# Kernel tuning notes

Hardware: AMD Instinct MI355X
Metric: run time of the kernel (lower is better)

The kernel has to match this reference:

```python
import jax, jax.numpy as jnp
import numpy as np

TROPICAL_ZERO = jnp.float32(-1e38)  # tropical additive identity (acts as -inf)


def setup_inputs() -> dict:
    key = jax.random.key(0)
    k_x, k_w = jax.random.split(key)
    B, IN, OUT = 4096, 256, 256
    x = jax.random.normal(k_x, (B, IN), dtype=jnp.float32)
    # weight = log(rand + 1e-6), matching nn.Parameter init in the torch module
    weight = jnp.log(jax.random.uniform(k_w, (OUT, IN), dtype=jnp.float32) + 1e-6)
    bias = jnp.zeros((OUT,), dtype=jnp.float32)
    return {"x": x, "weight": weight, "bias": bias}


def reference(x, weight, bias):
    # Tropical (max-plus) matmul: out[b, j] = max_k (x[b, k] + w[j, k]) + bias[j]
    # restricted to 'non-tropical-zero' products; if all products are tropical
    # zero, the output stays TROPICAL_ZERO (no bias added), as in the torch loop.
    products = x[:, None, :] + weight[None, :, :]          # [B, out, in]
    mask = products > TROPICAL_ZERO                        # [B, out, in]
    masked = jnp.where(mask, products, -jnp.inf)
    max_val = jnp.max(masked, axis=-1)                     # [B, out]
    any_valid = jnp.any(mask, axis=-1)                     # [B, out]
    out = jnp.where(any_valid, max_val + bias[None, :], TROPICAL_ZERO)
    return out
```

## Files before the change

kernel.cpp:

```cpp
#include <hip/hip_runtime.h>


#define TZERO -1e38f

constexpr int K     = 256;
constexpr int N     = 256;
constexpr int RPW   = 4;
constexpr int WAVES = 4;
constexpr int BM    = RPW * WAVES;
constexpr int BN    = 64;
constexpr int NT    = 64 * WAVES;
constexpr int BK    = 64;
constexpr int NC    = K / BK;
constexpr int K4C   = BK / 4;

__global__ __launch_bounds__(NT, 4)
void tropical_kernel(const float* __restrict__ x, const float* __restrict__ w,
                     const float* __restrict__ bias, float* __restrict__ out)
{
    __shared__ float4 wQ[2][K4C][BN];

    const int t    = threadIdx.x;
    const int lane = t & 63;
    const int wave = __builtin_amdgcn_readfirstlane(t >> 6);
    const int row0 = blockIdx.x * BM + wave * RPW;
    const int col0 = blockIdx.y * BN;

    const int scol = t & 63;
    const int sq   = t >> 6;
    const float* wsrc = w + (size_t)(col0 + scol) * K + sq * 16;

#pragma unroll
    for (int i = 0; i < 4; ++i)
        wQ[0][sq * 4 + i][scol] =
            *reinterpret_cast<const float4*>(wsrc + i * 4);
    __syncthreads();

    const float* xw = x + (size_t)row0 * K;

    float acc[RPW];
#pragma unroll
    for (int r = 0; r < RPW; ++r) acc[r] = -__builtin_inff();

    for (int c = 0; c < NC; ++c) {
        if (c + 1 < NC) {
            const float* ws = wsrc + (c + 1) * BK;
#pragma unroll
            for (int i = 0; i < 4; ++i)
                wQ[(c + 1) & 1][sq * 4 + i][scol] =
                    *reinterpret_cast<const float4*>(ws + i * 4);
        }

        const float* xc = xw + c * BK;
#pragma unroll 8
        for (int k4 = 0; k4 < K4C; ++k4) {
            const float4 wv = wQ[c & 1][k4][lane];
#pragma unroll
            for (int r = 0; r < RPW; ++r) {
                const float4 xv =
                    *reinterpret_cast<const float4*>(xc + r * K + k4 * 4);
                const float t0 = xv.x + wv.x;
                const float t1 = xv.y + wv.y;
                const float t2 = xv.z + wv.z;
                const float t3 = xv.w + wv.w;
                float m = fmaxf(fmaxf(acc[r], t0), t1);
                m       = fmaxf(fmaxf(m, t2), t3);
                acc[r] = m;
            }
        }
        __syncthreads();
    }

    const float bj = bias[col0 + lane];
    float* orow = out + (size_t)row0 * N + col0 + lane;
#pragma unroll
    for (int r = 0; r < RPW; ++r) {
        const float v = acc[r];
        orow[(size_t)r * N] = (v > TZERO) ? v + bj : TZERO;
    }
}

extern "C" void kernel_launch(void* const* d_in, const int* in_sizes, int n_in,
                              void* d_out, int out_size, void* d_ws, size_t ws_size,
                              hipStream_t stream) {
    const float* x  = (const float*)d_in[0];
    const float* w  = (const float*)d_in[1];
    const float* b  = (const float*)d_in[2];
    float* out      = (float*)d_out;

    dim3 grid(4096 / BM, N / BN);
    tropical_kernel<<<grid, NT, 0, stream>>>(x, w, b, out);
}
```

Before: 71.80 us.

## Split K across waves with register-resident weights and LDS max reduction

Each of the four waves now owns a quarter of the K dimension and keeps its 64-wide weight slice in registers (16 float4), instead of streaming weight chunks through double-buffered LDS. Each wave processes all 16 rows of the block, and the partial maxima are combined through a small shared array after one barrier. Two independent max chains per row add instruction-level parallelism. This removes the per-chunk LDS weight traffic and barriers, but costs higher register pressure (64 VGPRs for weights) and extra LDS work for the cross-wave reduction.

```diff
diff --git a/kernel.cpp b/kernel.cpp
--- a/kernel.cpp
+++ b/kernel.cpp
@@ -3,80 +3,65 @@
 
 #define TZERO -1e38f
 
-constexpr int K     = 256;
-constexpr int N     = 256;
-constexpr int RPW   = 4;
-constexpr int WAVES = 4;
-constexpr int BM    = RPW * WAVES;
-constexpr int BN    = 64;
-constexpr int NT    = 64 * WAVES;
-constexpr int BK    = 64;
-constexpr int NC    = K / BK;
-constexpr int K4C   = BK / 4;
+constexpr int K    = 256;
+constexpr int N    = 256;
+constexpr int ROWS = 16;
+constexpr int NT   = 256;
 
 __global__ __launch_bounds__(NT, 4)
 void tropical_kernel(const float* __restrict__ x, const float* __restrict__ w,
                      const float* __restrict__ bias, float* __restrict__ out)
 {
-    __shared__ float4 wQ[2][K4C][BN];
+    __shared__ float part[4][ROWS][64];
 
     const int t    = threadIdx.x;
     const int lane = t & 63;
-    const int wave = __builtin_amdgcn_readfirstlane(t >> 6);
-    const int row0 = blockIdx.x * BM + wave * RPW;
-    const int col0 = blockIdx.y * BN;
+    const int kq   = __builtin_amdgcn_readfirstlane(t >> 6);
+    const int row0 = blockIdx.x * ROWS;
+    const int col0 = blockIdx.y * 64;
 
-    const int scol = t & 63;
-    const int sq   = t >> 6;
-    const float* wsrc = w + (size_t)(col0 + scol) * K + sq * 16;
+    const float* wsrc = w + (size_t)(col0 + lane) * K + kq * 64;
+    float4 wq[16];
+#pragma unroll
+    for (int i = 0; i < 16; ++i)
+        wq[i] = *reinterpret_cast<const float4*>(wsrc + 4 * i);
 
+    const float bj = bias[col0 + lane];
+
+    const float* xbase = x + (size_t)row0 * K + kq * 64;
+
+#pragma unroll 2
+    for (int r = 0; r < ROWS; ++r) {
+        const float* xr = xbase + (size_t)r * K;
+        float m0 = -__builtin_inff();
+        float m1 = -__builtin_inff();
 #pragma unroll
-    for (int i = 0; i < 4; ++i)
-        wQ[0][sq * 4 + i][scol] =
-            *reinterpret_cast<const float4*>(wsrc + i * 4);
+        for (int i = 0; i < 16; ++i) {
+            const float4 xv = *reinterpret_cast<const float4*>(xr + 4 * i);
+            const float t0 = xv.x + wq[i].x;
+            const float t1 = xv.y + wq[i].y;
+            const float t2 = xv.z + wq[i].z;
+            const float t3 = xv.w + wq[i].w;
+            if (i & 1) {
+                m1 = fmaxf(fmaxf(m1, t0), t1);
+                m1 = fmaxf(fmaxf(m1, t2), t3);
+            } else {
+                m0 = fmaxf(fmaxf(m0, t0), t1);
+                m0 = fmaxf(fmaxf(m0, t2), t3);
+            }
+        }
+        part[kq][r][lane] = fmaxf(m0, m1);
+    }
+
     __syncthreads();
 
-    const float* xw = x + (size_t)row0 * K;
-
-    float acc[RPW];
+    const int er0 = (t >> 6) * 4;
 #pragma unroll
-    for (int r = 0; r < RPW; ++r) acc[r] = -__builtin_inff();
-
-    for (int c = 0; c < NC; ++c) {
-        if (c + 1 < NC) {
-            const float* ws = wsrc + (c + 1) * BK;
-#pragma unroll
-            for (int i = 0; i < 4; ++i)
-                wQ[(c + 1) & 1][sq * 4 + i][scol] =
-                    *reinterpret_cast<const float4*>(ws + i * 4);
-        }
-
-        const float* xc = xw + c * BK;
-#pragma unroll 8
-        for (int k4 = 0; k4 < K4C; ++k4) {
-            const float4 wv = wQ[c & 1][k4][lane];
-#pragma unroll
-            for (int r = 0; r < RPW; ++r) {
-                const float4 xv =
-                    *reinterpret_cast<const float4*>(xc + r * K + k4 * 4);
-                const float t0 = xv.x + wv.x;
-                const float t1 = xv.y + wv.y;
-                const float t2 = xv.z + wv.z;
-                const float t3 = xv.w + wv.w;
-                float m = fmaxf(fmaxf(acc[r], t0), t1);
-                m       = fmaxf(fmaxf(m, t2), t3);
-                acc[r] = m;
-            }
-        }
-        __syncthreads();
-    }
-
-    const float bj = bias[col0 + lane];
-    float* orow = out + (size_t)row0 * N + col0 + lane;
-#pragma unroll
-    for (int r = 0; r < RPW; ++r) {
-        const float v = acc[r];
-        orow[(size_t)r * N] = (v > TZERO) ? v + bj : TZERO;
+    for (int i = 0; i < 4; ++i) {
+        const int r = er0 + i;
+        const float v = fmaxf(fmaxf(part[0][r][lane], part[1][r][lane]),
+                              fmaxf(part[2][r][lane], part[3][r][lane]));
+        out[(size_t)(row0 + r) * N + col0 + lane] = (v > TZERO) ? v + bj : TZERO;
     }
 }
 
@@ -88,6 +73,6 @@
     const float* b  = (const float*)d_in[2];
     float* out      = (float*)d_out;
 
-    dim3 grid(4096 / BM, N / BN);
+    dim3 grid(4096 / ROWS, N / 64);
     tropical_kernel<<<grid, NT, 0, stream>>>(x, w, b, out);
 }
```

New measurement: 91.99 us. +28.1%, slower.
